# Kernel tuning notes

Hardware: AMD Instinct MI355X
Metric: run time of the kernel (lower is better)

Reference implementation:

```python
import jax, jax.numpy as jnp
import numpy as np
from jax.ops import segment_sum, segment_max

DIM = 64
NUM_FEAT = 14
EDGE_FEAT = 4
OUT_DIM = 16
NUM_GRAPHS = 512
NEG_SLOPE = 0.01


def _leaky(v):
    return jnp.where(v >= 0, v, NEG_SLOPE * v)


def setup_inputs() -> dict:
    key = jax.random.key(0)
    ks = jax.random.split(key, 24)
    N, E = 20000, 40000
    s = 0.1
    inp = {
        "x": jax.random.normal(ks[0], (N, NUM_FEAT), jnp.float32),
        "edge_attr": jax.random.normal(ks[1], (E, EDGE_FEAT), jnp.float32),
        "edge_index": jax.random.randint(ks[2], (2, E), 0, N, jnp.int64) if jax.config.jax_enable_x64 else jax.random.randint(ks[2], (2, E), 0, N).astype(jnp.int32),
        "batch": jnp.sort(jax.random.randint(ks[3], (N,), 0, NUM_GRAPHS)).astype(jnp.int32),
        # lin0
        "lin0_w": s * jax.random.normal(ks[4], (DIM, NUM_FEAT), jnp.float32),
        "lin0_b": s * jax.random.normal(ks[5], (DIM,), jnp.float32),
        # edge network: Linear(4,dim) -> LeakyReLU -> Linear(dim, dim*dim)
        "net_w1": s * jax.random.normal(ks[6], (DIM, EDGE_FEAT), jnp.float32),
        "net_b1": s * jax.random.normal(ks[7], (DIM,), jnp.float32),
        "net_w2": s * jax.random.normal(ks[8], (DIM * DIM, DIM), jnp.float32),
        "net_b2": s * jax.random.normal(ks[9], (DIM * DIM,), jnp.float32),
        # NNConv root weight + bias
        "root_w": s * jax.random.normal(ks[10], (DIM, DIM), jnp.float32),
        "conv_b": s * jax.random.normal(ks[11], (DIM,), jnp.float32),
        # GRU (torch gate order: r, z, n)
        "gru_w_ih": s * jax.random.normal(ks[12], (3 * DIM, DIM), jnp.float32),
        "gru_w_hh": s * jax.random.normal(ks[13], (3 * DIM, DIM), jnp.float32),
        "gru_b_ih": s * jax.random.normal(ks[14], (3 * DIM,), jnp.float32),
        "gru_b_hh": s * jax.random.normal(ks[15], (3 * DIM,), jnp.float32),
        # Set2Set LSTM (input 2*dim, hidden dim; torch gate order: i, f, g, o)
        "lstm_w_ih": s * jax.random.normal(ks[16], (4 * DIM, 2 * DIM), jnp.float32),
        "lstm_w_hh": s * jax.random.normal(ks[17], (4 * DIM, DIM), jnp.float32),
        "lstm_b_ih": s * jax.random.normal(ks[18], (4 * DIM,), jnp.float32),
        "lstm_b_hh": s * jax.random.normal(ks[19], (4 * DIM,), jnp.float32),
        # lin_out
        "lout_w": s * jax.random.normal(ks[20], (OUT_DIM, 2 * DIM), jnp.float32),
        "lout_b": s * jax.random.normal(ks[21], (OUT_DIM,), jnp.float32),
    }
    return inp


def _forward(x, edge_attr, lin0_w, lin0_b, net_w1, net_b1, net_w2, net_b2,
             root_w, conv_b, gru_w_ih, gru_w_hh, gru_b_ih, gru_b_hh,
             lstm_w_ih, lstm_w_hh, lstm_b_ih, lstm_b_hh, lout_w, lout_b,
             edge_index, batch):
    N = x.shape[0]
    src, tgt = edge_index[0], edge_index[1]

    # per-edge dim x dim weight (shared across the 6 steps; edge_attr is static)
    ew = _leaky(edge_attr @ net_w1.T + net_b1) @ net_w2.T + net_b2  # [E, dim*dim]
    ew = ew.reshape(-1, DIM, DIM)  # [E, in, out]

    deg = segment_sum(jnp.ones_like(tgt, jnp.float32), tgt, num_segments=N)
    inv_deg = 1.0 / jnp.maximum(deg, 1.0)

    out = _leaky(x @ lin0_w.T + lin0_b)  # [N, dim]
    h = out
    for _ in range(6):
        msg = jnp.einsum('ed,edo->eo', out[src], ew)  # gather + per-edge matvec
        agg = segment_sum(msg, tgt, num_segments=N) * inv_deg[:, None]  # scatter-mean
        conv = agg + out @ root_w + conv_b
        m = _leaky(conv)
        # GRU cell (seq len 1)
        gi = m @ gru_w_ih.T + gru_b_ih
        gh = h @ gru_w_hh.T + gru_b_hh
        gi_r, gi_z, gi_n = jnp.split(gi, 3, axis=-1)
        gh_r, gh_z, gh_n = jnp.split(gh, 3, axis=-1)
        r = jax.nn.sigmoid(gi_r + gh_r)
        z = jax.nn.sigmoid(gi_z + gh_z)
        n = jnp.tanh(gi_n + r * gh_n)
        h = (1.0 - z) * n + z * h
        out = h

    # Set2Set, processing_steps=1
    B = NUM_GRAPHS
    q_star = jnp.zeros((B, 2 * DIM), x.dtype)
    h_l = jnp.zeros((B, DIM), x.dtype)
    c_l = jnp.zeros((B, DIM), x.dtype)
    gates = q_star @ lstm_w_ih.T + lstm_b_ih + h_l @ lstm_w_hh.T + lstm_b_hh
    gi_, gf_, gg_, go_ = jnp.split(gates, 4, axis=-1)
    i_g = jax.nn.sigmoid(gi_)
    f_g = jax.nn.sigmoid(gf_)
    g_g = jnp.tanh(gg_)
    o_g = jax.nn.sigmoid(go_)
    c = f_g * c_l + i_g * g_g
    q = o_g * jnp.tanh(c)  # [B, dim]

    e = jnp.sum(out * q[batch], axis=-1)  # [N]
    emax = segment_max(e, batch, num_segments=B)
    emax = jnp.where(jnp.isfinite(emax), emax, 0.0)
    ex = jnp.exp(e - emax[batch])
    denom = segment_sum(ex, batch, num_segments=B)
    a = ex / jnp.maximum(denom, 1e-16)[batch]
    r_read = segment_sum(a[:, None] * out, batch, num_segments=B)  # [B, dim]
    q_star = jnp.concatenate([q, r_read], axis=-1)  # [B, 2*dim]

    return q_star @ lout_w.T + lout_b  # [B, out_dim]


def reference(x, edge_attr, edge_index, batch, lin0_w, lin0_b, net_w1, net_b1,
              net_w2, net_b2, root_w, conv_b, gru_w_ih, gru_w_hh, gru_b_ih,
              gru_b_hh, lstm_w_ih, lstm_w_hh, lstm_b_ih, lstm_b_hh, lout_w, lout_b):
    return _forward(x, edge_attr, lin0_w, lin0_b, net_w1, net_b1, net_w2, net_b2,
                    root_w, conv_b, gru_w_ih, gru_w_hh, gru_b_ih, gru_b_hh,
                    lstm_w_ih, lstm_w_hh, lstm_b_ih, lstm_b_hh, lout_w, lout_b,
                    edge_index, batch)
```

## Files before the change

### kernel.cpp

```cpp
#include <hip/hip_runtime.h>
#include <math.h>

#define DIM 64
#define NFEAT 14
#define EFEAT 4
#define ODIM 16
#define NGRAPH 512
#define NEG 0.01f
#define EBLK 128

typedef _Float16 f16;
typedef _Float16 f16x8 __attribute__((ext_vector_type(8)));
typedef float f32x4 __attribute__((ext_vector_type(4)));

#define MFMA(a,b,c) __builtin_amdgcn_mfma_f32_16x16x32_f16(a,b,c,0,0,0)

__device__ __forceinline__ float leaky(float v){ return v >= 0.f ? v : NEG*v; }
__device__ __forceinline__ float sigm(float v){ return 1.f/(1.f+expf(-v)); }

__global__ void k_pack(const float* __restrict__ src, f16* __restrict__ dst, int NC, int transB){
    int i = blockIdx.x*blockDim.x + threadIdx.x;
    if (i >= NC*64) return;
    int j = i & 7, l = (i >> 3) & 63, s = (i >> 9) & 1, CT = i >> 10;
    int k = ((l >> 4) << 3) + 32*s + j;
    int c = CT*16 + (l & 15);
    float v = transB ? src[(size_t)k*NC + c] : src[(size_t)c*64 + k];
    dst[i] = (f16)v;
}

__global__ void k_hid(const float* __restrict__ ea, const float* __restrict__ w1,
                      const float* __restrict__ b1, f16* __restrict__ hid16, int E){
    int i = blockIdx.x*blockDim.x + threadIdx.x;
    if (i >= E*DIM) return;
    int e = i >> 6, k = i & 63;
    const float* a = ea + (size_t)e*EFEAT;
    const float* w = w1 + k*EFEAT;
    float v = b1[k] + a[0]*w[0] + a[1]*w[1] + a[2]*w[2] + a[3]*w[3];
    hid16[i] = (f16)leaky(v);
}

__global__ void k_deg(const int* __restrict__ ei, float* __restrict__ deg, int E){
    int e = blockIdx.x*blockDim.x + threadIdx.x;
    if (e < E) atomicAdd(&deg[ei[E + e]], 1.0f);
}

__global__ void k_invdeg(float* __restrict__ deg, int N){
    int i = blockIdx.x*blockDim.x + threadIdx.x;
    if (i < N) deg[i] = 1.0f / fmaxf(deg[i], 1.0f);
}

__global__ void k_lin0(const float* __restrict__ x, const float* __restrict__ w,
                       const float* __restrict__ b, float* __restrict__ hf,
                       f16* __restrict__ out16, int N){
    int i = blockIdx.x*blockDim.x + threadIdx.x;
    if (i >= N*DIM) return;
    int n = i >> 6, o = i & 63;
    const float* xr = x + (size_t)n*NFEAT;
    const float* wr = w + o*NFEAT;
    float v = b[o];
#pragma unroll
    for (int f = 0; f < NFEAT; ++f) v += xr[f]*wr[f];
    v = leaky(v);
    hf[i] = v; out16[i] = (f16)v;
}

__global__ __launch_bounds__(256) void k_nbias(const f16x8* __restrict__ out16v,
                                               const f16x8* __restrict__ b2f,
                                               float* __restrict__ nb, int N){
    int n0 = blockIdx.x*64;
    int tid = threadIdx.x, w = tid >> 6, l = tid & 63, li = l & 15, lh = l >> 4;
    int ar = n0 + 16*w + li;
    f16x8 a0{}, a1{};
    if (ar < N){ a0 = out16v[(size_t)ar*8 + lh]; a1 = out16v[(size_t)ar*8 + lh + 4]; }
    f32x4 z = {0.f,0.f,0.f,0.f};
#pragma unroll
    for (int ct = 0; ct < 4; ++ct){
        f32x4 p = MFMA(a0, b2f[(ct*2+0)*64 + l], z);
        p = MFMA(a1, b2f[(ct*2+1)*64 + l], p);
#pragma unroll
        for (int reg = 0; reg < 4; ++reg){
            int n = n0 + 16*w + lh*4 + reg;
            if (n < N) nb[(size_t)n*64 + ct*16 + li] = p[reg];
        }
    }
}

__global__ __launch_bounds__(256) void k_fmsg(const float* __restrict__ hf,
                                              const f16x8* __restrict__ hid16v,
                                              const f16x8* __restrict__ wpf,
                                              const float* __restrict__ nb,
                                              const int* __restrict__ ei,
                                              float* __restrict__ agg, int E){
    __shared__ float Os[EBLK][65];
    __shared__ f16x8 Wch[4*512];
    __shared__ int ssrc[EBLK];
    __shared__ int stgt[EBLK];
    int tid = threadIdx.x;
    int e0 = blockIdx.x*EBLK;
    if (tid < EBLK){
        int e = e0 + tid;
        ssrc[tid] = (e < E) ? ei[e] : -1;
        stgt[tid] = (e < E) ? ei[E + e] : -1;
    }
    __syncthreads();
    for (int i = tid; i < EBLK*16; i += 256){
        int row = i >> 4, c4 = i & 15;
        int s = ssrc[row];
        float4 v = make_float4(0.f,0.f,0.f,0.f);
        if (s >= 0) v = *(const float4*)(hf + (size_t)s*64 + c4*4);
        *(float4*)&Os[row][c4*4] = v;
    }

    int w = tid >> 6, l = tid & 63, li = l & 15, lh = l >> 4;
    f16x8 a[2][2];
#pragma unroll
    for (int rt = 0; rt < 2; ++rt){
        int e = e0 + w*32 + rt*16 + li;
        if (e < E){
            a[rt][0] = hid16v[(size_t)e*8 + lh];
            a[rt][1] = hid16v[(size_t)e*8 + lh + 4];
        } else { a[rt][0] = f16x8{}; a[rt][1] = f16x8{}; }
    }

    float acc[2][4][4] = {};
    f32x4 z = {0.f,0.f,0.f,0.f};

    for (int g = 0; g < 16; ++g){
        __syncthreads();
        const f16x8* srcp = wpf + (size_t)g*2048;
        for (int i = tid; i < 2048; i += 256) Wch[i] = srcp[i];
        __syncthreads();
#pragma unroll
        for (int dd = 0; dd < 4; ++dd){
            int d = g*4 + dd;
            f16x8 b[4][2];
#pragma unroll
            for (int ct = 0; ct < 4; ++ct){
                b[ct][0] = Wch[dd*512 + (ct*2+0)*64 + l];
                b[ct][1] = Wch[dd*512 + (ct*2+1)*64 + l];
            }
            float osv[2][4];
#pragma unroll
            for (int rt = 0; rt < 2; ++rt)
#pragma unroll
                for (int reg = 0; reg < 4; ++reg)
                    osv[rt][reg] = Os[w*32 + rt*16 + lh*4 + reg][d];
#pragma unroll
            for (int rt = 0; rt < 2; ++rt){
#pragma unroll
                for (int ct = 0; ct < 4; ++ct){
                    f32x4 p = MFMA(a[rt][0], b[ct][0], z);
                    p = MFMA(a[rt][1], b[ct][1], p);
#pragma unroll
                    for (int reg = 0; reg < 4; ++reg)
                        acc[rt][ct][reg] += osv[rt][reg]*p[reg];
                }
            }
        }
    }

#pragma unroll
    for (int rt = 0; rt < 2; ++rt){
#pragma unroll
        for (int reg = 0; reg < 4; ++reg){
            int row = w*32 + rt*16 + lh*4 + reg;
            int t = stgt[row];
            if (t < 0) continue;
            int s = ssrc[row];
#pragma unroll
            for (int ct = 0; ct < 4; ++ct){
                int col = ct*16 + li;
                float v = acc[rt][ct][reg] + nb[(size_t)s*64 + col];
                atomicAdd(&agg[(size_t)t*64 + col], v);
            }
        }
    }
}

__global__ __launch_bounds__(256) void k_node(float* __restrict__ hf,
                                              f16* __restrict__ out16,
                                              const f16x8* __restrict__ out16v,
                                              const float* __restrict__ agg,
                                              const float* __restrict__ invdeg,
                                              const float* __restrict__ convb,
                                              const f16x8* __restrict__ wrf,
                                              const f16x8* __restrict__ wihf,
                                              const f16x8* __restrict__ whhf,
                                              const float* __restrict__ bih,
                                              const float* __restrict__ bhh, int N){
    __shared__ f16 Ms[64][72];
    int n0 = blockIdx.x*64;
    int tid = threadIdx.x, w = tid >> 6, l = tid & 63, li = l & 15, lh = l >> 4;
    f32x4 z = {0.f,0.f,0.f,0.f};

    int ar = n0 + 16*w + li;
    f16x8 a0{}, a1{};
    if (ar < N){ a0 = out16v[(size_t)ar*8 + lh]; a1 = out16v[(size_t)ar*8 + lh + 4]; }

    int nrow[4]; float invd[4];
#pragma unroll
    for (int reg = 0; reg < 4; ++reg){
        nrow[reg] = n0 + 16*w + lh*4 + reg;
        invd[reg] = (nrow[reg] < N) ? invdeg[nrow[reg]] : 0.f;
    }

#pragma unroll
    for (int ct = 0; ct < 4; ++ct){
        f32x4 p = MFMA(a0, wrf[(ct*2+0)*64 + l], z);
        p = MFMA(a1, wrf[(ct*2+1)*64 + l], p);
        int col = ct*16 + li;
        float cb = convb[col];
#pragma unroll
        for (int reg = 0; reg < 4; ++reg){
            int n = nrow[reg];
            float m = 0.f;
            if (n < N) m = leaky(p[reg] + agg[(size_t)n*64 + col]*invd[reg] + cb);
            Ms[16*w + lh*4 + reg][col] = (f16)m;
        }
    }
    __syncthreads();

    f16x8 am0 = *(const f16x8*)&Ms[16*w + li][lh*8];
    f16x8 am1 = *(const f16x8*)&Ms[16*w + li][lh*8 + 32];

#pragma unroll
    for (int ctq = 0; ctq < 4; ++ctq){
        int col = ctq*16 + li;
        f32x4 pir = MFMA(am0, wihf[((ctq+0)*2+0)*64 + l], z);
        pir = MFMA(am1, wihf[((ctq+0)*2+1)*64 + l], pir);
        f32x4 piz = MFMA(am0, wihf[((ctq+4)*2+0)*64 + l], z);
        piz = MFMA(am1, wihf[((ctq+4)*2+1)*64 + l], piz);
        f32x4 pin = MFMA(am0, wihf[((ctq+8)*2+0)*64 + l], z);
        pin = MFMA(am1, wihf[((ctq+8)*2+1)*64 + l], pin);
        f32x4 phr = MFMA(a0, whhf[((ctq+0)*2+0)*64 + l], z);
        phr = MFMA(a1, whhf[((ctq+0)*2+1)*64 + l], phr);
        f32x4 phz = MFMA(a0, whhf[((ctq+4)*2+0)*64 + l], z);
        phz = MFMA(a1, whhf[((ctq+4)*2+1)*64 + l], phz);
        f32x4 phn = MFMA(a0, whhf[((ctq+8)*2+0)*64 + l], z);
        phn = MFMA(a1, whhf[((ctq+8)*2+1)*64 + l], phn);
        float bir = bih[col], biz = bih[64+col], bin = bih[128+col];
        float bhr = bhh[col], bhz = bhh[64+col], bhn = bhh[128+col];
#pragma unroll
        for (int reg = 0; reg < 4; ++reg){
            int n = nrow[reg];
            if (n >= N) continue;
            float hv = hf[(size_t)n*64 + col];
            float r  = sigm(pir[reg] + bir + phr[reg] + bhr);
            float zz = sigm(piz[reg] + biz + phz[reg] + bhz);
            float nn = tanhf(pin[reg] + bin + r*(phn[reg] + bhn));
            float hnew = (1.f - zz)*nn + zz*hv;
            hf[(size_t)n*64 + col] = hnew;
            out16[(size_t)n*64 + col] = (f16)hnew;
        }
    }
}

__global__ void k_q(const float* __restrict__ bih, const float* __restrict__ bhh,
                    float* __restrict__ q){
    int j = threadIdx.x;
    if (j >= 64) return;
    float gi = bih[j]       + bhh[j];
    float gg = bih[128+j]   + bhh[128+j];
    float go = bih[192+j]   + bhh[192+j];
    float c = sigm(gi)*tanhf(gg);
    q[j] = sigm(go)*tanhf(c);
}

__device__ __forceinline__ unsigned fkey(float f){
    unsigned u = __float_as_uint(f);
    return (u >> 31) ? ~u : (u | 0x80000000u);
}

__global__ void k_edot(const float* __restrict__ out, const float* __restrict__ q,
                       const int* __restrict__ batch, float* __restrict__ ebuf,
                       unsigned* __restrict__ emaxk, int N){
    int gw = (blockIdx.x*blockDim.x + threadIdx.x) >> 6;
    int d = threadIdx.x & 63;
    if (gw >= N) return;
    float v = out[(size_t)gw*64 + d] * q[d];
#pragma unroll
    for (int s = 32; s; s >>= 1) v += __shfl_xor(v, s, 64);
    if (d == 0){
        ebuf[gw] = v;
        atomicMax(&emaxk[batch[gw]], fkey(v));
    }
}

__global__ void k_ex(float* __restrict__ ebuf, const unsigned* __restrict__ emaxk,
                     const int* __restrict__ batch, float* __restrict__ denom, int N){
    int n = blockIdx.x*blockDim.x + threadIdx.x;
    if (n >= N) return;
    int b = batch[n];
    unsigned k = emaxk[b];
    float em = (k == 0u) ? 0.f
             : ((k >> 31) ? __uint_as_float(k ^ 0x80000000u) : __uint_as_float(~k));
    float ex = expf(ebuf[n] - em);
    ebuf[n] = ex;
    atomicAdd(&denom[b], ex);
}

__global__ void k_rr(const float* __restrict__ out, const float* __restrict__ ebuf,
                     const float* __restrict__ denom, const int* __restrict__ batch,
                     float* __restrict__ rr, int N){
    int gw = (blockIdx.x*blockDim.x + threadIdx.x) >> 6;
    int o = threadIdx.x & 63;
    if (gw >= N) return;
    int b = batch[gw];
    float a = ebuf[gw] / fmaxf(denom[b], 1e-16f);
    atomicAdd(&rr[(size_t)b*64 + o], a * out[(size_t)gw*64 + o]);
}

__global__ void k_out(const float* __restrict__ q, const float* __restrict__ rr,
                      const float* __restrict__ lw, const float* __restrict__ lb,
                      float* __restrict__ dout){
    int i = blockIdx.x*blockDim.x + threadIdx.x;
    if (i >= NGRAPH*ODIM) return;
    int b = i / ODIM, j = i % ODIM;
    const float* w = lw + j*128;
    float acc = lb[j];
#pragma unroll 8
    for (int d = 0; d < 64; ++d) acc += w[d]*q[d];
    const float* rb = rr + (size_t)b*64;
#pragma unroll 8
    for (int d = 0; d < 64; ++d) acc += w[64+d]*rb[d];
    dout[i] = acc;
}

extern "C" void kernel_launch(void* const* d_in, const int* in_sizes, int n_in,
                              void* d_out, int out_size, void* d_ws, size_t ws_size,
                              hipStream_t stream){
    const float* x     = (const float*)d_in[0];
    const float* ea    = (const float*)d_in[1];
    const int*   ei    = (const int*)  d_in[2];
    const int*   batch = (const int*)  d_in[3];
    const float* lin0w = (const float*)d_in[4];
    const float* lin0b = (const float*)d_in[5];
    const float* w1    = (const float*)d_in[6];
    const float* b1    = (const float*)d_in[7];
    const float* w2    = (const float*)d_in[8];
    const float* b2    = (const float*)d_in[9];
    const float* rootw = (const float*)d_in[10];
    const float* convb = (const float*)d_in[11];
    const float* gwih  = (const float*)d_in[12];
    const float* gwhh  = (const float*)d_in[13];
    const float* gbih  = (const float*)d_in[14];
    const float* gbhh  = (const float*)d_in[15];
    const float* lsbih = (const float*)d_in[18];
    const float* lsbhh = (const float*)d_in[19];
    const float* loutw = (const float*)d_in[20];
    const float* loutb = (const float*)d_in[21];

    int N = in_sizes[0] / NFEAT;
    int E = in_sizes[1] / EFEAT;

    char* p = (char*)d_ws;
    size_t off = 0;
    auto carve = [&](size_t bytes) -> void* {
        void* r = p + off;
        off += (bytes + 255) & ~(size_t)255;
        return r;
    };
    f16*      hid16  = (f16*)     carve((size_t)E*64*2);
    float*    hf     = (float*)   carve((size_t)N*64*4);
    f16*      out16  = (f16*)     carve((size_t)N*64*2);
    float*    agg    = (float*)   carve((size_t)N*64*4);
    float*    nb     = (float*)   carve((size_t)N*64*4);
    float*    invdeg = (float*)   carve((size_t)N*4);
    float*    qv     = (float*)   carve(64*4);
    float*    ebuf   = (float*)   carve((size_t)N*4);
    unsigned* emaxk  = (unsigned*)carve(NGRAPH*4);
    float*    denom  = (float*)   carve(NGRAPH*4);
    float*    rr     = (float*)   carve((size_t)NGRAPH*64*4);
    f16*      wpf    = (f16*)     carve((size_t)4096*64*2);
    f16*      wrf    = (f16*)     carve(64*64*2);
    f16*      b2f    = (f16*)     carve(64*64*2);
    f16*      wihf   = (f16*)     carve(192*64*2);
    f16*      whhf   = (f16*)     carve(192*64*2);

    hipMemsetAsync(invdeg, 0, (size_t)N*4, stream);
    hipMemsetAsync(emaxk, 0, NGRAPH*4, stream);
    hipMemsetAsync(denom, 0, NGRAPH*4, stream);
    hipMemsetAsync(rr,    0, (size_t)NGRAPH*64*4, stream);

    k_pack<<<(4096*64 + 255)/256, 256, 0, stream>>>(w2,    wpf,  4096, 0);
    k_pack<<<(64*64   + 255)/256, 256, 0, stream>>>(rootw, wrf,  64,   1);
    k_pack<<<(64*64   + 255)/256, 256, 0, stream>>>(b2,    b2f,  64,   1);
    k_pack<<<(192*64  + 255)/256, 256, 0, stream>>>(gwih,  wihf, 192,  0);
    k_pack<<<(192*64  + 255)/256, 256, 0, stream>>>(gwhh,  whhf, 192,  0);

    k_hid<<<((size_t)E*64 + 255)/256, 256, 0, stream>>>(ea, w1, b1, hid16, E);
    k_deg<<<(E + 255)/256, 256, 0, stream>>>(ei, invdeg, E);
    k_invdeg<<<(N + 255)/256, 256, 0, stream>>>(invdeg, N);
    k_lin0<<<((size_t)N*64 + 255)/256, 256, 0, stream>>>(x, lin0w, lin0b, hf, out16, N);

    int eb  = (E + EBLK - 1)/EBLK;
    int nbk = (N + 63)/64;
    int node_grid = ((size_t)N*64 + 255)/256;
    for (int it = 0; it < 6; ++it){
        hipMemsetAsync(agg, 0, (size_t)N*64*4, stream);
        k_nbias<<<nbk, 256, 0, stream>>>((const f16x8*)out16, (const f16x8*)b2f, nb, N);
        k_fmsg<<<eb, 256, 0, stream>>>(hf, (const f16x8*)hid16, (const f16x8*)wpf,
                                       nb, ei, agg, E);
        k_node<<<nbk, 256, 0, stream>>>(hf, out16, (const f16x8*)out16, agg, invdeg,
                                        convb, (const f16x8*)wrf, (const f16x8*)wihf,
                                        (const f16x8*)whhf, gbih, gbhh, N);
    }

    k_q<<<1, 64, 0, stream>>>(lsbih, lsbhh, qv);
    k_edot<<<node_grid, 256, 0, stream>>>(hf, qv, batch, ebuf, emaxk, N);
    k_ex<<<(N + 255)/256, 256, 0, stream>>>(ebuf, emaxk, batch, denom, N);
    k_rr<<<node_grid, 256, 0, stream>>>(hf, ebuf, denom, batch, rr, N);
    k_out<<<(NGRAPH*ODIM + 255)/256, 256, 0, stream>>>(qv, rr, loutw, loutb, (float*)d_out);
}
```

Baseline: 589.0 us.

## Split edge-message kernel over feature dimension and fuse node-bias and zeroing into node kernel

The edge-message kernel is split across four slices of the source-feature dimension using a second grid axis. This raises the block count from about 313 to about 1250, so more CUs are kept busy. Each block now reads its weight rows directly from global memory instead of staging all 64 through shared memory. The per-iteration memset of agg and the separate node-bias kernel are folded into the node kernel, which zeroes agg after reading it and computes the next nb from the new hidden state. In exchange, global atomics to agg grow fourfold, and weight reads no longer go through shared memory.

```diff
diff --git a/kernel.cpp b/kernel.cpp
--- a/kernel.cpp
+++ b/kernel.cpp
@@ -8,6 +8,7 @@
 #define NGRAPH 512
 #define NEG 0.01f
 #define EBLK 128
+#define DSPLIT 4
 
 typedef _Float16 f16;
 typedef _Float16 f16x8 __attribute__((ext_vector_type(8)));
@@ -91,12 +92,13 @@
                                               const float* __restrict__ nb,
                                               const int* __restrict__ ei,
                                               float* __restrict__ agg, int E){
-    __shared__ float Os[EBLK][65];
-    __shared__ f16x8 Wch[4*512];
+    __shared__ float Os[EBLK][20];
     __shared__ int ssrc[EBLK];
     __shared__ int stgt[EBLK];
     int tid = threadIdx.x;
     int e0 = blockIdx.x*EBLK;
+    int dz = blockIdx.y;
+    int d0 = dz*16;
     if (tid < EBLK){
         int e = e0 + tid;
         ssrc[tid] = (e < E) ? ei[e] : -1;
@@ -104,11 +106,9 @@
     }
     __syncthreads();
     for (int i = tid; i < EBLK*16; i += 256){
-        int row = i >> 4, c4 = i & 15;
+        int row = i >> 4, dl = i & 15;
         int s = ssrc[row];
-        float4 v = make_float4(0.f,0.f,0.f,0.f);
-        if (s >= 0) v = *(const float4*)(hf + (size_t)s*64 + c4*4);
-        *(float4*)&Os[row][c4*4] = v;
+        Os[row][dl] = (s >= 0) ? hf[(size_t)s*64 + d0 + dl] : 0.f;
     }
 
     int w = tid >> 6, l = tid & 63, li = l & 15, lh = l >> 4;
@@ -121,40 +121,35 @@
             a[rt][1] = hid16v[(size_t)e*8 + lh + 4];
         } else { a[rt][0] = f16x8{}; a[rt][1] = f16x8{}; }
     }
+    __syncthreads();
 
     float acc[2][4][4] = {};
     f32x4 z = {0.f,0.f,0.f,0.f};
 
-    for (int g = 0; g < 16; ++g){
-        __syncthreads();
-        const f16x8* srcp = wpf + (size_t)g*2048;
-        for (int i = tid; i < 2048; i += 256) Wch[i] = srcp[i];
-        __syncthreads();
-#pragma unroll
-        for (int dd = 0; dd < 4; ++dd){
-            int d = g*4 + dd;
-            f16x8 b[4][2];
+#pragma unroll 2
+    for (int dd = 0; dd < 16; ++dd){
+        const f16x8* wrow = wpf + ((size_t)(d0 + dd))*512;
+        f16x8 b[4][2];
+#pragma unroll
+        for (int ct = 0; ct < 4; ++ct){
+            b[ct][0] = wrow[(ct*2+0)*64 + l];
+            b[ct][1] = wrow[(ct*2+1)*64 + l];
+        }
+        float osv[2][4];
+#pragma unroll
+        for (int rt = 0; rt < 2; ++rt)
+#pragma unroll
+            for (int reg = 0; reg < 4; ++reg)
+                osv[rt][reg] = Os[w*32 + rt*16 + lh*4 + reg][dd];
+#pragma unroll
+        for (int rt = 0; rt < 2; ++rt){
 #pragma unroll
             for (int ct = 0; ct < 4; ++ct){
-                b[ct][0] = Wch[dd*512 + (ct*2+0)*64 + l];
-                b[ct][1] = Wch[dd*512 + (ct*2+1)*64 + l];
-            }
-            float osv[2][4];
-#pragma unroll
-            for (int rt = 0; rt < 2; ++rt)
+                f32x4 p = MFMA(a[rt][0], b[ct][0], z);
+                p = MFMA(a[rt][1], b[ct][1], p);
 #pragma unroll
                 for (int reg = 0; reg < 4; ++reg)
-                    osv[rt][reg] = Os[w*32 + rt*16 + lh*4 + reg][d];
-#pragma unroll
-            for (int rt = 0; rt < 2; ++rt){
-#pragma unroll
-                for (int ct = 0; ct < 4; ++ct){
-                    f32x4 p = MFMA(a[rt][0], b[ct][0], z);
-                    p = MFMA(a[rt][1], b[ct][1], p);
-#pragma unroll
-                    for (int reg = 0; reg < 4; ++reg)
-                        acc[rt][ct][reg] += osv[rt][reg]*p[reg];
-                }
+                    acc[rt][ct][reg] += osv[rt][reg]*p[reg];
             }
         }
     }
@@ -170,7 +165,8 @@
 #pragma unroll
             for (int ct = 0; ct < 4; ++ct){
                 int col = ct*16 + li;
-                float v = acc[rt][ct][reg] + nb[(size_t)s*64 + col];
+                float v = acc[rt][ct][reg];
+                if (dz == 0) v += nb[(size_t)s*64 + col];
                 atomicAdd(&agg[(size_t)t*64 + col], v);
             }
         }
@@ -180,14 +176,16 @@
 __global__ __launch_bounds__(256) void k_node(float* __restrict__ hf,
                                               f16* __restrict__ out16,
                                               const f16x8* __restrict__ out16v,
-                                              const float* __restrict__ agg,
+                                              float* __restrict__ agg,
                                               const float* __restrict__ invdeg,
                                               const float* __restrict__ convb,
                                               const f16x8* __restrict__ wrf,
                                               const f16x8* __restrict__ wihf,
                                               const f16x8* __restrict__ whhf,
                                               const float* __restrict__ bih,
-                                              const float* __restrict__ bhh, int N){
+                                              const float* __restrict__ bhh,
+                                              const f16x8* __restrict__ b2f,
+                                              float* __restrict__ nb, int N){
     __shared__ f16 Ms[64][72];
     int n0 = blockIdx.x*64;
     int tid = threadIdx.x, w = tid >> 6, l = tid & 63, li = l & 15, lh = l >> 4;
@@ -214,7 +212,11 @@
         for (int reg = 0; reg < 4; ++reg){
             int n = nrow[reg];
             float m = 0.f;
-            if (n < N) m = leaky(p[reg] + agg[(size_t)n*64 + col]*invd[reg] + cb);
+            if (n < N){
+                size_t idx = (size_t)n*64 + col;
+                m = leaky(p[reg] + agg[idx]*invd[reg] + cb);
+                agg[idx] = 0.f;
+            }
             Ms[16*w + lh*4 + reg][col] = (f16)m;
         }
     }
@@ -240,17 +242,35 @@
         phn = MFMA(a1, whhf[((ctq+8)*2+1)*64 + l], phn);
         float bir = bih[col], biz = bih[64+col], bin = bih[128+col];
         float bhr = bhh[col], bhz = bhh[64+col], bhn = bhh[128+col];
+        __syncthreads();
 #pragma unroll
         for (int reg = 0; reg < 4; ++reg){
             int n = nrow[reg];
-            if (n >= N) continue;
-            float hv = hf[(size_t)n*64 + col];
-            float r  = sigm(pir[reg] + bir + phr[reg] + bhr);
-            float zz = sigm(piz[reg] + biz + phz[reg] + bhz);
-            float nn = tanhf(pin[reg] + bin + r*(phn[reg] + bhn));
-            float hnew = (1.f - zz)*nn + zz*hv;
-            hf[(size_t)n*64 + col] = hnew;
-            out16[(size_t)n*64 + col] = (f16)hnew;
+            float hnew = 0.f;
+            if (n < N){
+                float hv = hf[(size_t)n*64 + col];
+                float r  = sigm(pir[reg] + bir + phr[reg] + bhr);
+                float zz = sigm(piz[reg] + biz + phz[reg] + bhz);
+                float nn = tanhf(pin[reg] + bin + r*(phn[reg] + bhn));
+                hnew = (1.f - zz)*nn + zz*hv;
+                hf[(size_t)n*64 + col] = hnew;
+                out16[(size_t)n*64 + col] = (f16)hnew;
+            }
+            Ms[16*w + lh*4 + reg][col] = (f16)hnew;
+        }
+    }
+    __syncthreads();
+
+    f16x8 an0 = *(const f16x8*)&Ms[16*w + li][lh*8];
+    f16x8 an1 = *(const f16x8*)&Ms[16*w + li][lh*8 + 32];
+#pragma unroll
+    for (int ct = 0; ct < 4; ++ct){
+        f32x4 p = MFMA(an0, b2f[(ct*2+0)*64 + l], z);
+        p = MFMA(an1, b2f[(ct*2+1)*64 + l], p);
+#pragma unroll
+        for (int reg = 0; reg < 4; ++reg){
+            int n = nrow[reg];
+            if (n < N) nb[(size_t)n*64 + ct*16 + li] = p[reg];
         }
     }
 }
@@ -381,6 +401,7 @@
     hipMemsetAsync(emaxk, 0, NGRAPH*4, stream);
     hipMemsetAsync(denom, 0, NGRAPH*4, stream);
     hipMemsetAsync(rr,    0, (size_t)NGRAPH*64*4, stream);
+    hipMemsetAsync(agg,   0, (size_t)N*64*4, stream);
 
     k_pack<<<(4096*64 + 255)/256, 256, 0, stream>>>(w2,    wpf,  4096, 0);
     k_pack<<<(64*64   + 255)/256, 256, 0, stream>>>(rootw, wrf,  64,   1);
@@ -396,14 +417,15 @@
     int eb  = (E + EBLK - 1)/EBLK;
     int nbk = (N + 63)/64;
     int node_grid = ((size_t)N*64 + 255)/256;
+
+    k_nbias<<<nbk, 256, 0, stream>>>((const f16x8*)out16, (const f16x8*)b2f, nb, N);
     for (int it = 0; it < 6; ++it){
-        hipMemsetAsync(agg, 0, (size_t)N*64*4, stream);
-        k_nbias<<<nbk, 256, 0, stream>>>((const f16x8*)out16, (const f16x8*)b2f, nb, N);
-        k_fmsg<<<eb, 256, 0, stream>>>(hf, (const f16x8*)hid16, (const f16x8*)wpf,
-                                       nb, ei, agg, E);
+        k_fmsg<<<dim3(eb, DSPLIT), 256, 0, stream>>>(hf, (const f16x8*)hid16,
+                                                     (const f16x8*)wpf, nb, ei, agg, E);
         k_node<<<nbk, 256, 0, stream>>>(hf, out16, (const f16x8*)out16, agg, invdeg,
                                         convb, (const f16x8*)wrf, (const f16x8*)wihf,
-                                        (const f16x8*)whhf, gbih, gbhh, N);
+                                        (const f16x8*)whhf, gbih, gbhh,
+                                        (const f16x8*)b2f, nb, N);
     }
 
     k_q<<<1, 64, 0, stream>>>(lsbih, lsbhh, qv);
```

Result: no change. 590.0 us (+0.2%).
